# Performance work log

Hardware: AMD Instinct MI355X
Metric: run time of the kernel (lower is better)

The kernel has to match this reference:

```python
import jax, jax.numpy as jnp
import numpy as np
import math

# Fixed representative draw of the host-side RNG (all aug probs fired).
MIRROR_X, MIRROR_Y = -1.0, 1.0      # x flip on, y flip off
TX, TY = 0.06, -0.04                # translate percents
SX, SY = 1.1, 0.95                  # anisotropic scale
ZOOM = 0.9                          # isotropic zoom (draws from params['scale'] range in source)
ROT = math.radians(27.0)            # rotate degrees -> rad
SHX, SHY = 0.05, -0.03              # shear percents


def _affine_grid(theta, H, W):
    # torch F.affine_grid with align_corners=False: pixel-center normalized coords
    xs = (jnp.arange(W, dtype=jnp.float32) + 0.5) * (2.0 / W) - 1.0
    ys = (jnp.arange(H, dtype=jnp.float32) + 0.5) * (2.0 / H) - 1.0
    gx, gy = jnp.meshgrid(xs, ys)  # [H,W]
    coords = jnp.stack([gx, gy, jnp.ones_like(gx)], axis=-1)  # [H,W,3]
    return jnp.einsum('ij,hwj->hwi', theta, coords)  # [H,W,2] (x,y); same grid for all batch


def _gather(img, iy, ix, valid):
    # img [B,C,H,W]; iy/ix [H,W] int32; valid [H,W] bool. zeros padding.
    B, C, H, W = img.shape
    idx = (jnp.clip(iy, 0, H - 1) * W + jnp.clip(ix, 0, W - 1)).reshape(-1)
    g = img.reshape(B, C, H * W)[:, :, idx].reshape(B, C, H, W)
    return jnp.where(valid[None, None], g, jnp.zeros((), img.dtype))


def _unnormalize(grid, H, W):
    # align_corners=False unnormalization
    ix = ((grid[..., 0] + 1.0) * W - 1.0) * 0.5
    iy = ((grid[..., 1] + 1.0) * H - 1.0) * 0.5
    return ix, iy


def _grid_sample_bilinear(img, grid):
    B, C, H, W = img.shape
    ix, iy = _unnormalize(grid, H, W)
    x0 = jnp.floor(ix); y0 = jnp.floor(iy)
    wx1 = ix - x0; wx0 = 1.0 - wx1
    wy1 = iy - y0; wy0 = 1.0 - wy1
    x0i = x0.astype(jnp.int32); y0i = y0.astype(jnp.int32)
    x1i = x0i + 1; y1i = y0i + 1
    inb = lambda x, y: (x >= 0) & (x < W) & (y >= 0) & (y < H)
    v00 = _gather(img, y0i, x0i, inb(x0i, y0i))
    v01 = _gather(img, y0i, x1i, inb(x1i, y0i))
    v10 = _gather(img, y1i, x0i, inb(x0i, y1i))
    v11 = _gather(img, y1i, x1i, inb(x1i, y1i))
    out = (v00 * (wy0 * wx0)[None, None] + v01 * (wy0 * wx1)[None, None]
           + v10 * (wy1 * wx0)[None, None] + v11 * (wy1 * wx1)[None, None])
    return out


def _grid_sample_nearest(img, grid):
    B, C, H, W = img.shape
    ix, iy = _unnormalize(grid, H, W)
    xi = jnp.round(ix).astype(jnp.int32)
    yi = jnp.round(iy).astype(jnp.int32)
    valid = (xi >= 0) & (xi < W) & (yi >= 0) & (yi < H)
    return _gather(img, yi, xi, valid)


def _thetas():
    c, s = math.cos(ROT), math.sin(ROT)
    return [
        jnp.array([[MIRROR_X, 0.0, 0.0], [0.0, MIRROR_Y, 0.0]], jnp.float32),  # mirror
        jnp.array([[1.0, 0.0, TX], [0.0, 1.0, TY]], jnp.float32),              # translate
        jnp.array([[SX, 0.0, 0.0], [0.0, SY, 0.0]], jnp.float32),              # scale
        jnp.array([[ZOOM, 0.0, 0.0], [0.0, ZOOM, 0.0]], jnp.float32),          # zoom
        jnp.array([[c, -s, 0.0], [s, c, 0.0]], jnp.float32),                   # rotate
        jnp.array([[1.0, SHX, 0.0], [SHY, 1.0, 0.0]], jnp.float32),            # shear
    ]


def setup_inputs() -> dict:
    key = jax.random.key(0)
    k1, k2 = jax.random.split(key)
    img = jax.random.normal(k1, (16, 3, 512, 512), dtype=jnp.float32)
    label = jax.random.uniform(k2, (16, 3, 512, 512), dtype=jnp.float32)
    return {"img": img, "label": label}


def reference(img, label):
    B, C, H, W = img.shape
    # Sequential resampling, exactly as the torch module: one affine_grid +
    # grid_sample pair per enabled augmentation, bilinear for img / nearest for label.
    for theta in _thetas():
        grid = _affine_grid(theta, H, W)
        img = _grid_sample_bilinear(img, grid)
        label = _grid_sample_nearest(label, grid)
    return img, label
```

## Files before the change

kernel.cpp:

```cpp
#include <hip/hip_runtime.h>
#include <math.h>

#define HW 262144
#define TOTAL 12582912
#define TS 32
#define NT 512
#define P 3
#define NGROUP 16

#define CR 0.8910065241883679f
#define SR 0.45399049973954675f

#define K5CX (255.5f * (1.0f - CR + SR))
#define K5CY (255.5f * (1.0f - SR - CR))

#define W2 52
#define H2 44
#define W3 46
#define H3 45
#define W4 49
#define H4 48
#define W5 36
#define H5 35
#define BUFA_SZ 2352
#define BUFB_SZ 2070

struct Box { int x0, x1, y0, y1; };

__device__ __forceinline__ Box back_box(Box d, float A, float B, float C,
                                        float D, float E, float F) {
    float xa = (float)d.x0, xb = (float)d.x1, ya = (float)d.y0, yb = (float)d.y1;
    float mnx = fminf(A * xa, A * xb) + fminf(B * ya, B * yb) + C;
    float mxx = fmaxf(A * xa, A * xb) + fmaxf(B * ya, B * yb) + C;
    float mny = fminf(D * xa, D * xb) + fminf(E * ya, E * yb) + F;
    float mxy = fmaxf(D * xa, D * xb) + fmaxf(E * ya, E * yb) + F;
    Box s;
    s.x0 = (int)floorf(mnx); s.x1 = (int)floorf(mxx) + 1;
    s.y0 = (int)floorf(mny); s.y1 = (int)floorf(mxy) + 1;
    return s;
}

template <bool INT>
__device__ __forceinline__ void s2_eval(int i, const float* __restrict__ gin,
                                        float* __restrict__ dst, int rx0, int ry0)
{
    int ly = i / W2;
    int lx = i - ly * W2;
    int pxi = rx0 + lx, pyi = ry0 + ly;
    if (INT) {
        int off = ((pyi - 11) << 9) + (496 - pxi);
        #pragma unroll
        for (int p = 0; p < P; ++p) {
            const float* g0 = gin + p * HW + off;
            float v00 = g0[0], v01 = g0[-1];
            float v10 = g0[512], v11 = g0[511];
            float h0 = fmaf(0.36f, v01, 0.64f * v00);
            float h1 = fmaf(0.36f, v11, 0.64f * v10);
            dst[p * BUFA_SZ + i] = fmaf(0.76f, h1, 0.24f * h0);
        }
    } else {
        float wx0m = ((unsigned)pxi <= 496u) ? 0.64f : 0.0f;
        float wx1m = ((unsigned)pxi <= 495u) ? 0.36f : 0.0f;
        float wy0m = ((unsigned)(pyi - 11) <= 500u) ? 0.24f : 0.0f;
        float wy1m = ((unsigned)(pyi - 10) <= 501u) ? 0.76f : 0.0f;
        int xc0 = min(max(496 - pxi, 0), 511);
        int xc1 = min(max(495 - pxi, 0), 511);
        int r0 = min(max(pyi - 11, 0), 511) << 9;
        int r1 = min(max(pyi - 10, 0), 511) << 9;
        #pragma unroll
        for (int p = 0; p < P; ++p) {
            const float* g = gin + p * HW;
            float v00 = g[r0 + xc0], v01 = g[r0 + xc1];
            float v10 = g[r1 + xc0], v11 = g[r1 + xc1];
            float h0 = fmaf(wx1m, v01, wx0m * v00);
            float h1 = fmaf(wx1m, v11, wx0m * v10);
            dst[p * BUFA_SZ + i] = fmaf(wy1m, h1, wy0m * h0);
        }
    }
}

template <int SW, int SH, int DW, int SSTR, int DSTR, bool AXIS, bool INT>
__device__ __forceinline__ void lds_eval(int i, float A, float B, float Cs,
    float D, float E, float Fs, const float* __restrict__ src,
    float* __restrict__ dst, int dx0, int dy0)
{
    int ly = i / DW;
    int lx = i - ly * DW;
    int pxi = dx0 + lx, pyi = dy0 + ly;
    float px = (float)pxi, py = (float)pyi;
    float fx = AXIS ? fmaf(A, px, Cs) : fmaf(A, px, fmaf(B, py, Cs));
    float fy = AXIS ? fmaf(E, py, Fs) : fmaf(D, px, fmaf(E, py, Fs));
    float xf = floorf(fx), yf = floorf(fy);
    float wx = fx - xf, wy = fy - yf;
    int x0 = (int)xf, y0 = (int)yf;
    if (!INT) { x0 = min(max(x0, 0), SW - 2); y0 = min(max(y0, 0), SH - 2); }
    int sbase = y0 * SW + x0;
    bool oob = ((unsigned)pxi >= 512u || (unsigned)pyi >= 512u);
    #pragma unroll
    for (int p = 0; p < P; ++p) {
        const float* s = src + p * SSTR + sbase;
        float v00 = s[0], v01 = s[1];
        float v10 = s[SW], v11 = s[SW + 1];
        float a0 = fmaf(wx, v01 - v00, v00);
        float a1 = fmaf(wx, v11 - v10, v10);
        float val = fmaf(wy, a1 - a0, a0);
        if (!INT) { if (oob) val = 0.f; }
        dst[p * DSTR + i] = val;
    }
}

template <int SW, int SH, int DW, int DTOT, int SSTR, int DSTR, bool AXIS, bool INT>
__device__ __forceinline__ void stage_lds(int tid, float A, float B, float Cs,
    float D, float E, float Fs, const float* __restrict__ src,
    float* __restrict__ dst, int dx0, int dy0)
{
    constexpr int FULL = DTOT / NT;
    constexpr int TAIL = DTOT - FULL * NT;
    #pragma unroll
    for (int k = 0; k < FULL; ++k)
        lds_eval<SW, SH, DW, SSTR, DSTR, AXIS, INT>(tid + k * NT, A, B, Cs,
                                                    D, E, Fs, src, dst, dx0, dy0);
    if (TAIL && tid < TAIL)
        lds_eval<SW, SH, DW, SSTR, DSTR, AXIS, INT>(tid + FULL * NT, A, B, Cs,
                                                    D, E, Fs, src, dst, dx0, dy0);
}

template <bool INT>
__device__ __forceinline__ void s6_eval(int ii, const float* __restrict__ src,
    float* __restrict__ go, int tx0, int ty0, int sx0, int sy0)
{
    int lx = ii & 31, ly = ii >> 5;
    float px = (float)(tx0 + lx), py = (float)(ty0 + ly);
    float fx = fmaf(0.05f, py, -12.775f - (float)sx0) + px;
    float fy = fmaf(-0.03f, px, 7.665f - (float)sy0) + py;
    float xf = floorf(fx), yf = floorf(fy);
    float wx = fx - xf, wy = fy - yf;
    int x0 = (int)xf, y0 = (int)yf;
    if (!INT) { x0 = min(max(x0, 0), W5 - 2); y0 = min(max(y0, 0), H5 - 2); }
    int sbase = y0 * W5 + x0;
    int gidx = (ty0 + ly) * 512 + tx0 + lx;
    #pragma unroll
    for (int p = 0; p < P; ++p) {
        const float* s = src + p * BUFB_SZ + sbase;
        float v00 = s[0], v01 = s[1];
        float v10 = s[W5], v11 = s[W5 + 1];
        float a0 = fmaf(wx, v01 - v00, v00);
        float a1 = fmaf(wx, v11 - v10, v10);
        float val = fmaf(wy, a1 - a0, a0);
        __builtin_nontemporal_store(val, &go[p * HW + gidx]);
    }
}

template <bool INT>
__device__ __forceinline__ void img_tile(int tid, const float* __restrict__ gin,
    float* __restrict__ go, int tx0, int ty0,
    Box R2, Box R3, Box R4, Box R5, float* bufA, float* bufB)
{
    {
        constexpr int FULL = (W2 * H2) / NT;
        constexpr int TAIL = W2 * H2 - FULL * NT;
        #pragma unroll
        for (int k = 0; k < FULL; ++k)
            s2_eval<INT>(tid + k * NT, gin, bufA, R2.x0, R2.y0);
        if (tid < TAIL) s2_eval<INT>(tid + FULL * NT, gin, bufA, R2.x0, R2.y0);
    }
    __syncthreads();
    stage_lds<W2, H2, W3, W3 * H3, BUFA_SZ, BUFB_SZ, true, INT>(tid,
        1.1f, 0.0f, -25.55f - (float)R2.x0,
        0.0f, 0.95f, 12.775f - (float)R2.y0, bufA, bufB, R3.x0, R3.y0);
    __syncthreads();
    stage_lds<W3, H3, W4, W4 * H4, BUFB_SZ, BUFA_SZ, true, INT>(tid,
        0.9f, 0.0f, 25.55f - (float)R3.x0,
        0.0f, 0.9f, 25.55f - (float)R3.y0, bufB, bufA, R4.x0, R4.y0);
    __syncthreads();
    stage_lds<W4, H4, W5, W5 * H5, BUFA_SZ, BUFB_SZ, false, INT>(tid,
        CR, -SR, K5CX - (float)R4.x0,
        SR,  CR, K5CY - (float)R4.y0, bufA, bufB, R5.x0, R5.y0);
    __syncthreads();
    {
        constexpr int FULL = (TS * TS) / NT;
        #pragma unroll
        for (int k = 0; k < FULL; ++k)
            s6_eval<INT>(tid + k * NT, bufB, go, tx0, ty0, R5.x0, R5.y0);
    }
}

__global__ void compose_nearest_map(int* __restrict__ map) {
    int p = blockIdx.x * blockDim.x + threadIdx.x;
    if (p >= HW) return;
    const float TH[6][6] = {
        { 1.0f,  0.05f, 0.0f,  -0.03f, 1.0f,  0.0f },
        { CR,    -SR,   0.0f,   SR,    CR,    0.0f },
        { 0.9f,  0.0f,  0.0f,   0.0f,  0.9f,  0.0f },
        { 1.1f,  0.0f,  0.0f,   0.0f,  0.95f, 0.0f },
        { 1.0f,  0.0f,  0.06f,  0.0f,  1.0f, -0.04f },
        { -1.0f, 0.0f,  0.0f,   0.0f,  1.0f,  0.0f },
    };
    int cx = p & 511, cy = p >> 9;
    bool valid = true;
    #pragma unroll
    for (int s = 0; s < 6; ++s) {
        if (!valid) break;
        float x = (cx + 0.5f) * (2.0f / 512.0f) - 1.0f;
        float y = (cy + 0.5f) * (2.0f / 512.0f) - 1.0f;
        float gx = TH[s][0] * x + TH[s][1] * y + TH[s][2];
        float gy = TH[s][3] * x + TH[s][4] * y + TH[s][5];
        float ix = ((gx + 1.0f) * 512.0f - 1.0f) * 0.5f;
        float iy = ((gy + 1.0f) * 512.0f - 1.0f) * 0.5f;
        float xr = rintf(ix), yr = rintf(iy);
        if (xr < 0.0f || xr > 511.0f || yr < 0.0f || yr > 511.0f) valid = false;
        else { cx = (int)xr; cy = (int)yr; }
    }
    map[p] = valid ? (cy * 512 + cx) : -1;
}

__global__ __launch_bounds__(NT, 6) void fused_all(
    const float* __restrict__ img, const float* __restrict__ lab,
    const int* __restrict__ map, float* __restrict__ oimg,
    float* __restrict__ olab)
{
    __shared__ float bufA[P * BUFA_SZ];
    __shared__ float bufB[P * BUFB_SZ];
    int tid = threadIdx.x;
    int b = blockIdx.x;
    int group = b >> 8, tile = b & 255;
    int tx0 = (tile & 15) * TS, ty0 = (tile >> 4) * TS;
    int pbase = group * P;
    const float* gin = img + pbase * HW;
    const float* lin = lab + pbase * HW;
    float* go = oimg + pbase * HW;
    float* lo = olab + pbase * HW;

    {
        constexpr int FULL = (TS * TS) / NT;
        #pragma unroll
        for (int k = 0; k < FULL; ++k) {
            int ii = tid + k * NT;
            int gidx = (ty0 + (ii >> 5)) * 512 + tx0 + (ii & 31);
            int m = map[gidx];
            #pragma unroll
            for (int p = 0; p < P; ++p) {
                float v = (m >= 0) ? lin[p * HW + m] : 0.f;
                __builtin_nontemporal_store(v, &lo[p * HW + gidx]);
            }
        }
    }

    Box R6 = {tx0, tx0 + TS - 1, ty0, ty0 + TS - 1};
    Box R5 = back_box(R6, 1.0f, 0.05f, -12.775f, -0.03f, 1.0f, 7.665f);
    R5.x1 = min(R5.x1, R5.x0 + W5 - 1); R5.y1 = min(R5.y1, R5.y0 + H5 - 1);
    Box R4 = back_box(R5, CR, -SR, K5CX, SR, CR, K5CY);
    R4.x1 = min(R4.x1, R4.x0 + W4 - 1); R4.y1 = min(R4.y1, R4.y0 + H4 - 1);
    Box R3 = back_box(R4, 0.9f, 0.0f, 25.55f, 0.0f, 0.9f, 25.55f);
    R3.x1 = min(R3.x1, R3.x0 + W3 - 1); R3.y1 = min(R3.y1, R3.y0 + H3 - 1);
    Box R2 = back_box(R3, 1.1f, 0.0f, -25.55f, 0.0f, 0.95f, 12.775f);

    bool dead = (R2.x1 < 0 || R2.x0 > 511 || R2.y1 < 0 || R2.y0 > 511)
             || (R3.x1 < 0 || R3.x0 > 511 || R3.y1 < 0 || R3.y0 > 511)
             || (R4.x1 < 0 || R4.x0 > 511 || R4.y1 < 0 || R4.y0 > 511)
             || (R5.x1 < 0 || R5.x0 > 511 || R5.y1 < 0 || R5.y0 > 511);
    if (dead) {
        constexpr int FULL = (TS * TS) / NT;
        #pragma unroll
        for (int k = 0; k < FULL; ++k) {
            int ii = tid + k * NT;
            int gidx = (ty0 + (ii >> 5)) * 512 + tx0 + (ii & 31);
            #pragma unroll
            for (int p = 0; p < P; ++p)
                __builtin_nontemporal_store(0.f, &go[p * HW + gidx]);
        }
        return;
    }

    bool interior =
        R2.x0 >= 0 && R2.x0 + W2 - 1 <= 495 && R2.y0 >= 11 && R2.y0 + H2 - 1 <= 511 &&
        R3.x0 >= 0 && R3.x0 + W3 - 1 <= 511 && R3.y0 >= 0 && R3.y0 + H3 - 1 <= 511 &&
        R4.x0 >= 0 && R4.x0 + W4 - 1 <= 511 && R4.y0 >= 0 && R4.y0 + H4 - 1 <= 511 &&
        R5.x0 >= 0 && R5.x0 + W5 - 1 <= 511 && R5.y0 >= 0 && R5.y0 + H5 - 1 <= 511;

    if (interior)
        img_tile<true >(tid, gin, go, tx0, ty0, R2, R3, R4, R5, bufA, bufB);
    else
        img_tile<false>(tid, gin, go, tx0, ty0, R2, R3, R4, R5, bufA, bufB);
}

extern "C" void kernel_launch(void* const* d_in, const int* in_sizes, int n_in,
                              void* d_out, int out_size, void* d_ws, size_t ws_size,
                              hipStream_t stream) {
    const float* img_in = (const float*)d_in[0];
    const float* lab_in = (const float*)d_in[1];
    float* out_img = (float*)d_out;
    float* out_lab = (float*)d_out + TOTAL;
    int* map = (int*)d_ws;

    compose_nearest_map<<<(HW + 255) / 256, 256, 0, stream>>>(map);
    fused_all<<<NGROUP * 256, NT, 0, stream>>>(img_in, lab_in, map, out_img, out_lab);
}
```

Before: 78.12 us.

## Pack two planes per block as float2 in LDS to vectorize intermediate stages

```diff
diff --git a/kernel.cpp b/kernel.cpp
--- a/kernel.cpp
+++ b/kernel.cpp
@@ -5,8 +5,8 @@
 #define TOTAL 12582912
 #define TS 32
 #define NT 512
-#define P 3
-#define NGROUP 16
+#define P 2
+#define NGROUP 24
 
 #define CR 0.8910065241883679f
 #define SR 0.45399049973954675f
@@ -40,24 +40,36 @@
     return s;
 }
 
+__device__ __forceinline__ float2 lerp2(float w, float2 a, float2 b) {
+    float2 r;
+    r.x = fmaf(w, b.x - a.x, a.x);
+    r.y = fmaf(w, b.y - a.y, a.y);
+    return r;
+}
+
 template <bool INT>
 __device__ __forceinline__ void s2_eval(int i, const float* __restrict__ gin,
-                                        float* __restrict__ dst, int rx0, int ry0)
+                                        float2* __restrict__ dst, int rx0, int ry0)
 {
     int ly = i / W2;
     int lx = i - ly * W2;
     int pxi = rx0 + lx, pyi = ry0 + ly;
     if (INT) {
         int off = ((pyi - 11) << 9) + (496 - pxi);
-        #pragma unroll
-        for (int p = 0; p < P; ++p) {
-            const float* g0 = gin + p * HW + off;
-            float v00 = g0[0], v01 = g0[-1];
-            float v10 = g0[512], v11 = g0[511];
-            float h0 = fmaf(0.36f, v01, 0.64f * v00);
-            float h1 = fmaf(0.36f, v11, 0.64f * v10);
-            dst[p * BUFA_SZ + i] = fmaf(0.76f, h1, 0.24f * h0);
-        }
+        float2 o;
+        {
+            const float* g0 = gin + off;
+            float h0 = fmaf(0.36f, g0[-1], 0.64f * g0[0]);
+            float h1 = fmaf(0.36f, g0[511], 0.64f * g0[512]);
+            o.x = fmaf(0.76f, h1, 0.24f * h0);
+        }
+        {
+            const float* g1 = gin + HW + off;
+            float h0 = fmaf(0.36f, g1[-1], 0.64f * g1[0]);
+            float h1 = fmaf(0.36f, g1[511], 0.64f * g1[512]);
+            o.y = fmaf(0.76f, h1, 0.24f * h0);
+        }
+        dst[i] = o;
     } else {
         float wx0m = ((unsigned)pxi <= 496u) ? 0.64f : 0.0f;
         float wx1m = ((unsigned)pxi <= 495u) ? 0.36f : 0.0f;
@@ -67,6 +79,7 @@
         int xc1 = min(max(495 - pxi, 0), 511);
         int r0 = min(max(pyi - 11, 0), 511) << 9;
         int r1 = min(max(pyi - 10, 0), 511) << 9;
+        float2 o;
         #pragma unroll
         for (int p = 0; p < P; ++p) {
             const float* g = gin + p * HW;
@@ -74,15 +87,17 @@
             float v10 = g[r1 + xc0], v11 = g[r1 + xc1];
             float h0 = fmaf(wx1m, v01, wx0m * v00);
             float h1 = fmaf(wx1m, v11, wx0m * v10);
-            dst[p * BUFA_SZ + i] = fmaf(wy1m, h1, wy0m * h0);
-        }
-    }
-}
-
-template <int SW, int SH, int DW, int SSTR, int DSTR, bool AXIS, bool INT>
+            float val = fmaf(wy1m, h1, wy0m * h0);
+            if (p == 0) o.x = val; else o.y = val;
+        }
+        dst[i] = o;
+    }
+}
+
+template <int SW, int SH, int DW, bool AXIS, bool INT>
 __device__ __forceinline__ void lds_eval(int i, float A, float B, float Cs,
-    float D, float E, float Fs, const float* __restrict__ src,
-    float* __restrict__ dst, int dx0, int dy0)
+    float D, float E, float Fs, const float2* __restrict__ src,
+    float2* __restrict__ dst, int dx0, int dy0)
 {
     int ly = i / DW;
     int lx = i - ly * DW;
@@ -94,39 +109,36 @@
     float wx = fx - xf, wy = fy - yf;
     int x0 = (int)xf, y0 = (int)yf;
     if (!INT) { x0 = min(max(x0, 0), SW - 2); y0 = min(max(y0, 0), SH - 2); }
-    int sbase = y0 * SW + x0;
-    bool oob = ((unsigned)pxi >= 512u || (unsigned)pyi >= 512u);
-    #pragma unroll
-    for (int p = 0; p < P; ++p) {
-        const float* s = src + p * SSTR + sbase;
-        float v00 = s[0], v01 = s[1];
-        float v10 = s[SW], v11 = s[SW + 1];
-        float a0 = fmaf(wx, v01 - v00, v00);
-        float a1 = fmaf(wx, v11 - v10, v10);
-        float val = fmaf(wy, a1 - a0, a0);
-        if (!INT) { if (oob) val = 0.f; }
-        dst[p * DSTR + i] = val;
-    }
-}
-
-template <int SW, int SH, int DW, int DTOT, int SSTR, int DSTR, bool AXIS, bool INT>
+    const float2* s = src + y0 * SW + x0;
+    float2 v00 = s[0], v01 = s[1];
+    float2 v10 = s[SW], v11 = s[SW + 1];
+    float2 a0 = lerp2(wx, v00, v01);
+    float2 a1 = lerp2(wx, v10, v11);
+    float2 val = lerp2(wy, a0, a1);
+    if (!INT) {
+        if ((unsigned)pxi >= 512u || (unsigned)pyi >= 512u) { val.x = 0.f; val.y = 0.f; }
+    }
+    dst[i] = val;
+}
+
+template <int SW, int SH, int DW, int DTOT, bool AXIS, bool INT>
 __device__ __forceinline__ void stage_lds(int tid, float A, float B, float Cs,
-    float D, float E, float Fs, const float* __restrict__ src,
-    float* __restrict__ dst, int dx0, int dy0)
+    float D, float E, float Fs, const float2* __restrict__ src,
+    float2* __restrict__ dst, int dx0, int dy0)
 {
     constexpr int FULL = DTOT / NT;
     constexpr int TAIL = DTOT - FULL * NT;
     #pragma unroll
     for (int k = 0; k < FULL; ++k)
-        lds_eval<SW, SH, DW, SSTR, DSTR, AXIS, INT>(tid + k * NT, A, B, Cs,
-                                                    D, E, Fs, src, dst, dx0, dy0);
+        lds_eval<SW, SH, DW, AXIS, INT>(tid + k * NT, A, B, Cs, D, E, Fs,
+                                        src, dst, dx0, dy0);
     if (TAIL && tid < TAIL)
-        lds_eval<SW, SH, DW, SSTR, DSTR, AXIS, INT>(tid + FULL * NT, A, B, Cs,
-                                                    D, E, Fs, src, dst, dx0, dy0);
+        lds_eval<SW, SH, DW, AXIS, INT>(tid + FULL * NT, A, B, Cs, D, E, Fs,
+                                        src, dst, dx0, dy0);
 }
 
 template <bool INT>
-__device__ __forceinline__ void s6_eval(int ii, const float* __restrict__ src,
+__device__ __forceinline__ void s6_eval(int ii, const float2* __restrict__ src,
     float* __restrict__ go, int tx0, int ty0, int sx0, int sy0)
 {
     int lx = ii & 31, ly = ii >> 5;
@@ -137,24 +149,21 @@
     float wx = fx - xf, wy = fy - yf;
     int x0 = (int)xf, y0 = (int)yf;
     if (!INT) { x0 = min(max(x0, 0), W5 - 2); y0 = min(max(y0, 0), H5 - 2); }
-    int sbase = y0 * W5 + x0;
+    const float2* s = src + y0 * W5 + x0;
+    float2 v00 = s[0], v01 = s[1];
+    float2 v10 = s[W5], v11 = s[W5 + 1];
+    float2 a0 = lerp2(wx, v00, v01);
+    float2 a1 = lerp2(wx, v10, v11);
+    float2 val = lerp2(wy, a0, a1);
     int gidx = (ty0 + ly) * 512 + tx0 + lx;
-    #pragma unroll
-    for (int p = 0; p < P; ++p) {
-        const float* s = src + p * BUFB_SZ + sbase;
-        float v00 = s[0], v01 = s[1];
-        float v10 = s[W5], v11 = s[W5 + 1];
-        float a0 = fmaf(wx, v01 - v00, v00);
-        float a1 = fmaf(wx, v11 - v10, v10);
-        float val = fmaf(wy, a1 - a0, a0);
-        __builtin_nontemporal_store(val, &go[p * HW + gidx]);
-    }
+    __builtin_nontemporal_store(val.x, &go[gidx]);
+    __builtin_nontemporal_store(val.y, &go[HW + gidx]);
 }
 
 template <bool INT>
 __device__ __forceinline__ void img_tile(int tid, const float* __restrict__ gin,
     float* __restrict__ go, int tx0, int ty0,
-    Box R2, Box R3, Box R4, Box R5, float* bufA, float* bufB)
+    Box R2, Box R3, Box R4, Box R5, float2* bufA, float2* bufB)
 {
     {
         constexpr int FULL = (W2 * H2) / NT;
@@ -165,15 +174,15 @@
         if (tid < TAIL) s2_eval<INT>(tid + FULL * NT, gin, bufA, R2.x0, R2.y0);
     }
     __syncthreads();
-    stage_lds<W2, H2, W3, W3 * H3, BUFA_SZ, BUFB_SZ, true, INT>(tid,
+    stage_lds<W2, H2, W3, W3 * H3, true, INT>(tid,
         1.1f, 0.0f, -25.55f - (float)R2.x0,
         0.0f, 0.95f, 12.775f - (float)R2.y0, bufA, bufB, R3.x0, R3.y0);
     __syncthreads();
-    stage_lds<W3, H3, W4, W4 * H4, BUFB_SZ, BUFA_SZ, true, INT>(tid,
+    stage_lds<W3, H3, W4, W4 * H4, true, INT>(tid,
         0.9f, 0.0f, 25.55f - (float)R3.x0,
         0.0f, 0.9f, 25.55f - (float)R3.y0, bufB, bufA, R4.x0, R4.y0);
     __syncthreads();
-    stage_lds<W4, H4, W5, W5 * H5, BUFA_SZ, BUFB_SZ, false, INT>(tid,
+    stage_lds<W4, H4, W5, W5 * H5, false, INT>(tid,
         CR, -SR, K5CX - (float)R4.x0,
         SR,  CR, K5CY - (float)R4.y0, bufA, bufB, R5.x0, R5.y0);
     __syncthreads();
@@ -214,13 +223,13 @@
     map[p] = valid ? (cy * 512 + cx) : -1;
 }
 
-__global__ __launch_bounds__(NT, 6) void fused_all(
+__global__ __launch_bounds__(NT, 8) void fused_all(
     const float* __restrict__ img, const float* __restrict__ lab,
     const int* __restrict__ map, float* __restrict__ oimg,
     float* __restrict__ olab)
 {
-    __shared__ float bufA[P * BUFA_SZ];
-    __shared__ float bufB[P * BUFB_SZ];
+    __shared__ float2 bufA[BUFA_SZ];
+    __shared__ float2 bufB[BUFB_SZ];
     int tid = threadIdx.x;
     int b = blockIdx.x;
     int group = b >> 8, tile = b & 255;
@@ -238,11 +247,10 @@
             int ii = tid + k * NT;
             int gidx = (ty0 + (ii >> 5)) * 512 + tx0 + (ii & 31);
             int m = map[gidx];
-            #pragma unroll
-            for (int p = 0; p < P; ++p) {
-                float v = (m >= 0) ? lin[p * HW + m] : 0.f;
-                __builtin_nontemporal_store(v, &lo[p * HW + gidx]);
-            }
+            float v0 = (m >= 0) ? lin[m] : 0.f;
+            float v1 = (m >= 0) ? lin[HW + m] : 0.f;
+            __builtin_nontemporal_store(v0, &lo[gidx]);
+            __builtin_nontemporal_store(v1, &lo[HW + gidx]);
         }
     }
 
@@ -265,9 +273,8 @@
         for (int k = 0; k < FULL; ++k) {
             int ii = tid + k * NT;
             int gidx = (ty0 + (ii >> 5)) * 512 + tx0 + (ii & 31);
-            #pragma unroll
-            for (int p = 0; p < P; ++p)
-                __builtin_nontemporal_store(0.f, &go[p * HW + gidx]);
+            __builtin_nontemporal_store(0.f, &go[gidx]);
+            __builtin_nontemporal_store(0.f, &go[HW + gidx]);
         }
         return;
     }
```

New measurement: 67.86 us. 13.1% less time.
